# Optimization experiments

Measured on AMD Instinct MI355X. Metric: run time of the kernel, lower is better.

## Reference

```python
import jax, jax.numpy as jnp
import numpy as np
from jax import lax


def _l2n(t, eps=1e-12):
    n = jnp.sqrt(jnp.sum(t * t, axis=-1, keepdims=True))
    return t / jnp.maximum(n, eps)


def _ln(t, w, b, eps=1e-5):
    mu = jnp.mean(t, -1, keepdims=True)
    var = jnp.var(t, -1, keepdims=True)
    return (t - mu) / jnp.sqrt(var + eps) * w + b


def _unfold3(x):
    # nn.Unfold(kernel_size=3, padding=1, stride=1): [B,C,H,W] -> [B,C,9,H*W]
    B, C, H, W = x.shape
    xp = jnp.pad(x, ((0, 0), (0, 0), (1, 1), (1, 1)))
    pat = jnp.stack([xp[:, :, i:i + H, j:j + W] for i in range(3) for j in range(3)], axis=2)
    return pat.reshape(B, C, 9, H * W)


def _forward(x, norm1_w, norm1_b, q_w, q_b, kv_w, kv_b, temperature, query_embedding,
             learnable_tokens, learnable_bias, sr_w, sr_b, pln_w, pln_b, proj_w, proj_b,
             norm2_w, norm2_b, fc1_w, fc1_b, dw_w, dw_b, fc2_w, fc2_b):
    B, C, H, W = x.shape
    nh = temperature.shape[0]
    d = C // nh
    N = H * W
    K = 9  # local_len = window_size**2
    # norm1 (WithBias LayerNorm over channel dim, channels-last)
    y = _ln(x.reshape(B, C, N).transpose(0, 2, 1), norm1_w, norm1_b)  # [B,N,C]
    # ---- AggregatedAttention ----
    q = (y @ q_w.T + q_b).reshape(B, N, nh, d).transpose(0, 2, 1, 3)  # [B,h,N,d]
    qn = _l2n(q)
    qs = (qn + query_embedding) * jax.nn.softplus(temperature)
    kv = y @ kv_w.T + kv_b  # [B,N,2C]
    k_loc = _l2n(kv[..., :C].reshape(B, N, nh, d)).reshape(B, N, C)
    kvl = jnp.concatenate([k_loc, kv[..., C:]], -1).transpose(0, 2, 1).reshape(B, 2 * C, H, W)
    pat = _unfold3(kvl).reshape(B, 2 * nh, d, K, N).transpose(0, 1, 4, 2, 3)  # [B,2h,N,d,K]
    k_l, v_l = pat[:, :nh], pat[:, nh:]
    attn_local = jnp.einsum('bhnd,bhndk->bhnk', qs, k_l)  # [B,h,N,K]
    # pooled branch; sr_ratio=1 so adaptive_avg_pool2d is identity
    y4 = y.transpose(0, 2, 1).reshape(B, C, H, W)
    xp = jax.nn.gelu(jnp.einsum('oc,bchw->bohw', sr_w, y4) + sr_b[:, None, None], approximate=False)
    xp = _ln(xp.reshape(B, C, N).transpose(0, 2, 1), pln_w, pln_b)  # [B,pool_len,C]
    kvp = (xp @ kv_w.T + kv_b).reshape(B, N, 2 * nh, d).transpose(0, 2, 1, 3)
    k_p = _l2n(kvp[:, :nh])
    v_p = kvp[:, nh:]
    attn_pool = jnp.einsum('bhnd,bhmd->bhnm', qs, k_p)  # [B,h,N,pool_len]
    attn = jax.nn.softmax(jnp.concatenate([attn_local, attn_pool], -1), axis=-1)
    a_l, a_p = attn[..., :K], attn[..., K:]
    w_l = jnp.einsum('bhnd,hdk->bhnk', qn, learnable_tokens) + learnable_bias + a_l
    x_local = jnp.einsum('bhnk,bhndk->bhnd', w_l, v_l)
    x_pool = jnp.einsum('bhnm,bhmd->bhnd', a_p, v_p)
    xo = (x_local + x_pool).transpose(0, 2, 1, 3).reshape(B, N, C)
    # proj then raw torch-style reshape [B,N,C] -> [B,C,H,W] (memory reinterpretation)
    xo = (xo @ proj_w.T + proj_b).reshape(B, C, H, W)
    x = x + xo
    # ---- ConvolutionalGLU MLP ----
    hf = dw_b.shape[0]
    y2 = _ln(x.reshape(B, C, N).transpose(0, 2, 1), norm2_w, norm2_b).transpose(0, 2, 1).reshape(B, C, H, W)
    f1 = jnp.einsum('oc,bchw->bohw', fc1_w, y2) + fc1_b[:, None, None]
    a, v = f1[:, :hf], f1[:, hf:]
    dw = lax.conv_general_dilated(a, dw_w, (1, 1), ((1, 1), (1, 1)),
                                  feature_group_count=hf,
                                  dimension_numbers=('NCHW', 'OIHW', 'NCHW')) + dw_b[:, None, None]
    g = jax.nn.gelu(dw, approximate=False) * v
    out = jnp.einsum('oc,bchw->bohw', fc2_w, g) + fc2_b[:, None, None]
    return x + out


def setup_inputs() -> dict:
    key = jax.random.key(0)
    B, C, H, W = 2, 128, 56, 56
    nh, d, K = 4, 32, 9
    hf = int(2 * int(C * 4.0) / 3)  # 341
    ks = iter(jax.random.split(key, 16))
    rn = lambda shape, s=0.02: jax.random.normal(next(ks), shape, jnp.float32) * s
    return {
        'x': jax.random.normal(next(ks), (B, C, H, W), jnp.float32),
        'norm1_w': jnp.ones((C,), jnp.float32), 'norm1_b': jnp.zeros((C,), jnp.float32),
        'q_w': rn((C, C)), 'q_b': jnp.zeros((C,), jnp.float32),
        'kv_w': rn((2 * C, C)), 'kv_b': jnp.zeros((2 * C,), jnp.float32),
        'temperature': jnp.full((nh, 1, 1), float(np.log(np.exp(1.0 / 0.24) - 1.0)), jnp.float32),
        'query_embedding': rn((nh, 1, d)),
        'learnable_tokens': rn((nh, d, K)),
        'learnable_bias': jnp.zeros((nh, 1, K), jnp.float32),
        'sr_w': rn((C, C)), 'sr_b': jnp.zeros((C,), jnp.float32),
        'pln_w': jnp.ones((C,), jnp.float32), 'pln_b': jnp.zeros((C,), jnp.float32),
        'proj_w': rn((C, C)), 'proj_b': jnp.zeros((C,), jnp.float32),
        'norm2_w': jnp.ones((C,), jnp.float32), 'norm2_b': jnp.zeros((C,), jnp.float32),
        'fc1_w': rn((2 * hf, C)), 'fc1_b': jnp.zeros((2 * hf,), jnp.float32),
        'dw_w': rn((hf, 1, 3, 3)), 'dw_b': jnp.zeros((hf,), jnp.float32),
        'fc2_w': rn((C, hf)), 'fc2_b': jnp.zeros((C,), jnp.float32),
    }


def reference(x, norm1_w, norm1_b, q_w, q_b, kv_w, kv_b, temperature, query_embedding,
              learnable_tokens, learnable_bias, sr_w, sr_b, pln_w, pln_b, proj_w, proj_b,
              norm2_w, norm2_b, fc1_w, fc1_b, dw_w, dw_b, fc2_w, fc2_b):
    return _forward(x, norm1_w, norm1_b, q_w, q_b, kv_w, kv_b, temperature, query_embedding,
                    learnable_tokens, learnable_bias, sr_w, sr_b, pln_w, pln_b, proj_w, proj_b,
                    norm2_w, norm2_b, fc1_w, fc1_b, dw_w, dw_b, fc2_w, fc2_b)
```

## Files before the change

### kernel.cpp

```cpp
#include <hip/hip_runtime.h>
#include <hip/hip_bf16.h>

typedef __hip_bfloat16 bf16;
typedef short s8v __attribute__((ext_vector_type(8)));
typedef short s4v __attribute__((ext_vector_type(4)));
typedef float f4v __attribute__((ext_vector_type(4)));

#define DEVI __device__ __forceinline__

DEVI float cvt(float x){ return x; }
DEVI float cvt(bf16 x){ return __bfloat162float(x); }

DEVI void stg(float* p, float v){ *p = v; }
DEVI void stg(bf16* p, float v){ *p = __float2bfloat16(v); }

DEVI float gelu_exact(float x){
  return 0.5f*x*(1.0f + erff(x*0.70710678118654752440f));
}

constexpr int B_ = 2, C_ = 128, H_ = 56, W_ = 56, N_ = 3136, NH_ = 4, D_ = 32, HF_ = 341;
constexpr int ROWS_ = B_*N_;
constexpr int KF2 = 352;
constexpr int GQ_ = NH_*B_*N_;
constexpr int FW = 512;
constexpr int KSP = 12;
constexpr int SPLIT = 256;
constexpr int NTILE = 392;
constexpr float LOG2E = 1.4426950408889634f;
constexpr float E8L2  = 11.541560327111707f;

DEVI void ln_tile_body(int tile, int t, const float* __restrict__ x,
                       const float* __restrict__ w, const float* __restrict__ bia,
                       bf16* __restrict__ y, float* sm , float* st )
{
  int b = tile / 196, nb = (tile % 196) * 16;
  {
    int c = t >> 1, half = t & 1;
    const float* xp = x + ((long)b*C_ + c)*N_ + nb + half*8;
    f4v v0 = *(const f4v*)xp;
    f4v v1 = *(const f4v*)(xp + 4);
    #pragma unroll
    for (int j=0;j<4;j++){
      sm[c*17 + half*8 + j    ] = v0[j];
      sm[c*17 + half*8 + 4 + j] = v1[j];
    }
  }
  __syncthreads();
  {
    int i = t >> 4, k = t & 15;
    float s = 0.f, ss = 0.f;
    #pragma unroll
    for (int u=0;u<8;u++){
      float v = sm[(k + u*16)*17 + i];
      s += v; ss = fmaf(v,v,ss);
    }
    #pragma unroll
    for (int off=1; off<16; off<<=1){
      s  += __shfl_xor(s,  off);
      ss += __shfl_xor(ss, off);
    }
    if (k == 0){
      float mu  = s*(1.0f/128.0f);
      float var = fmaxf(ss*(1.0f/128.0f) - mu*mu, 0.f);
      st[i]      = mu;
      st[16 + i] = rsqrtf(var + 1e-5f);
    }
  }
  __syncthreads();
  {
    int i = t >> 4, c0 = (t & 15)*8;
    float mu = st[i], inv = st[16 + i];
    bf16 o8[8];
    #pragma unroll
    for (int j=0;j<8;j++){
      int c = c0 + j;
      o8[j] = __float2bfloat16((sm[c*17 + i] - mu)*inv*w[c] + bia[c]);
    }
    *(s8v*)(y + ((long)(b*N_ + nb + i))*C_ + c0) = *(const s8v*)o8;
  }
}

__global__ __launch_bounds__(256)
void ln_tile_kernel(const float* __restrict__ x, const float* __restrict__ w,
                    const float* __restrict__ bia, bf16* __restrict__ y)
{
  __shared__ float sm[128*17];
  __shared__ float st[32];
  ln_tile_body(blockIdx.x, threadIdx.x, x, w, bia, y, sm, st);
}

__global__ __launch_bounds__(256)
void head_kernel(const float* __restrict__ q_w, const float* __restrict__ kv_w,
                 const float* __restrict__ sr_w, const float* __restrict__ proj_w,
                 const float* __restrict__ fc1_w, const float* __restrict__ fc2_w,
                 const float* __restrict__ q_b, const float* __restrict__ kv_b,
                 const float* __restrict__ sr_b,
                 bf16* __restrict__ out, float* __restrict__ bias_out,
                 const float* __restrict__ x_in, const float* __restrict__ n1w,
                 const float* __restrict__ n1b, bf16* __restrict__ y)
{
  __shared__ float sm[128*17];
  __shared__ float st[32];
  if (blockIdx.x >= 839){
    ln_tile_body(blockIdx.x - 839, threadIdx.x, x_in, n1w, n1b, y, sm, st);
    return;
  }
  int t = blockIdx.x*256 + threadIdx.x;
  if (t >= 214272){
    int i = t - 214272;
    if (i < 512){
      float bv = (i < 128) ? q_b[i] : (i < 384) ? kv_b[i-128] : sr_b[i-384];
      bias_out[i] = bv;
    }
    return;
  }
  float v;
  if      (t <  16384) v = q_w[t];
  else if (t <  49152) v = kv_w[t-16384];
  else if (t <  65536) v = sr_w[t-49152];
  else if (t <  81920) v = proj_w[t-65536];
  else if (t < 169216) v = fc1_w[t-81920];
  else {
    int i = t - 169216; int m = i / KF2, kp = i % KF2;
    v = (kp < HF_) ? fc2_w[m*HF_ + kp] : 0.f;
  }
  out[t] = __float2bfloat16(v);
}

template<int KT, int MODE, typename TC, int BM=64, int LDA=KT, int NCH=1>
__global__ __launch_bounds__(256)
void gemm_mfma(const bf16* __restrict__ A, const bf16* __restrict__ B,
               const float* __restrict__ bias, const float* __restrict__ res,
               TC* __restrict__ Cm, int M, int Nn,
               long sA, long sB, long sC, long sR,
               const float* __restrict__ qe, const float* __restrict__ temp,
               bf16* __restrict__ aux0, bf16* __restrict__ aux1)
{
  A  += (long)blockIdx.z * sA;
  B  += (long)blockIdx.z * sB;
  Cm += (long)blockIdx.z * sC;
  if (res) res += (long)blockIdx.z * sR;
  int lane = threadIdx.x & 63, w = threadIdx.x >> 6;
  int m = lane & 15, quad = lane >> 4;
  int n0 = blockIdx.x*64, m0 = blockIdx.y*BM;
  const bf16* ap[NCH];
  #pragma unroll
  for (int cc=0; cc<NCH; cc++){
    int ar = m0 + cc*64 + w*16 + m;
    if (ar >= M) ar = M-1;
    ap[cc] = A + (long)ar*LDA + quad*8;
  }
  const bf16* bp = B + (long)(n0 + m)*KT + quad*8;
  s8v a4[KT/32];
  if (MODE==7){
    float s=0.f, ssum=0.f;
    #pragma unroll
    for (int i=0;i<KT/32;i++){
      a4[i] = *(const s8v*)(ap[0] + i*32);
      #pragma unroll
      for (int j=0;j<8;j++){
        float v = cvt(((const bf16*)&a4[i])[j]);
        s += v; ssum = fmaf(v,v,ssum);
      }
    }
    s    += __shfl_xor(s,16);    s    += __shfl_xor(s,32);
    ssum += __shfl_xor(ssum,16); ssum += __shfl_xor(ssum,32);
    float mu  = s*(1.0f/128.0f);
    float var = fmaxf(ssum*(1.0f/128.0f) - mu*mu, 0.f);
    float inv = rsqrtf(var + 1e-5f);
    #pragma unroll
    for (int i=0;i<KT/32;i++){
      #pragma unroll
      for (int j=0;j<8;j++){
        int c = i*32 + quad*8 + j;
        float v = cvt(((const bf16*)&a4[i])[j]);
        ((bf16*)&a4[i])[j] = __float2bfloat16((v-mu)*inv*qe[c] + temp[c]);
      }
    }
  }
  f4v acc[NCH][4];
  #pragma unroll
  for (int cc=0; cc<NCH; cc++)
    #pragma unroll
    for (int s=0;s<4;s++) acc[cc][s] = (f4v){0.f,0.f,0.f,0.f};
  #pragma unroll
  for (int k0 = 0; k0 < KT; k0 += 32){
    s8v bf[4];
    #pragma unroll
    for (int s=0;s<4;s++) bf[s] = *(const s8v*)(bp + (long)s*16*KT + k0);
    #pragma unroll
    for (int cc=0; cc<NCH; cc++){
      s8v af = (MODE==7) ? a4[k0/32] : *(const s8v*)(ap[cc] + k0);
      #pragma unroll
      for (int s=0;s<4;s++)
        acc[cc][s] = __builtin_amdgcn_mfma_f32_16x16x32_bf16(af, bf[s], acc[cc][s], 0, 0, 0);
    }
  }
  if ((MODE==6 || MODE==7) && blockIdx.x < 2){
    int hA = blockIdx.x*2, hB = hA+1;
    float spA = 0.f, spB = 0.f;
    if (MODE==6){
      spA = log1pf(expf(temp[hA])) * LOG2E;
      spB = log1pf(expf(temp[hB])) * LOG2E;
    }
    #pragma unroll
    for (int cc=0; cc<NCH; cc++){
      #pragma unroll
      for (int r=0;r<4;r++){
        float v4[4];
        #pragma unroll
        for (int s=0;s<4;s++) v4[s] = acc[cc][s][r] + bias[n0 + s*16 + m];
        float ssA = v4[0]*v4[0] + v4[1]*v4[1];
        float ssB = v4[2]*v4[2] + v4[3]*v4[3];
        #pragma unroll
        for (int off=1; off<16; off<<=1){
          ssA += __shfl_xor(ssA, off);
          ssB += __shfl_xor(ssB, off);
        }
        float invA = 1.f/fmaxf(sqrtf(ssA), 1e-12f);
        float invB = 1.f/fmaxf(sqrtf(ssB), 1e-12f);
        int gm = m0 + cc*64 + w*16 + quad*4 + r;
        int b = gm / N_, n = gm % N_;
        #pragma unroll
        for (int s=0;s<4;s++){
          int h = (s<2) ? hA : hB;
          int d = (s&1)*16 + m;
          float v = v4[s] * ((s<2) ? invA : invB);
          if (MODE==6) v = (v + qe[h*D_ + d]) * ((s<2) ? spA : spB);
          aux0[((long)(b*NH_+h)*N_ + n)*D_ + d] = __float2bfloat16(v);
        }
      }
    }
    return;
  }
  if (MODE==7){
    int gm0 = m0 + w*16 + quad*4;
    int b = gm0 / N_, nb = gm0 % N_;
    #pragma unroll
    for (int s=0;s<4;s++){
      int h = (blockIdx.x-2)*2 + (s>>1);
      int d = (s&1)*16 + m;
      bf16 p4[4];
      #pragma unroll
      for (int r=0;r<4;r++) p4[r] = __float2bfloat16(acc[0][s][r] + bias[n0 + s*16 + m]);
      *(s4v*)(aux1 + ((long)(b*NH_+h)*D_ + d)*N_ + nb) = *(const s4v*)p4;
    }
    return;
  }
  #pragma unroll
  for (int cc=0; cc<NCH; cc++){
    int m0c = m0 + cc*64;
    #pragma unroll
    for (int s=0;s<4;s++){
      int gn = n0 + s*16 + m;
      #pragma unroll
      for (int r=0;r<4;r++){
        int gm = m0c + w*16 + quad*4 + r;
        if (gm >= M) continue;
        float v = acc[cc][s][r];
        if (MODE==1 || MODE==4 || MODE==6) v += bias[gn];
        else                               v += bias[gm];
        if (MODE==6 && gn >= 384) v = gelu_exact(v);
        if (MODE==4 || MODE==5) v += res[(long)gm*Nn + gn];
        stg(&Cm[(long)gm*Nn + gn], v);
      }
    }
  }
}

__global__ __launch_bounds__(256)
void attn_part_kernel(const bf16* __restrict__ qs_, const bf16* __restrict__ kp_,
                      const bf16* __restrict__ vp_,
                      bf16* __restrict__ Op, float* __restrict__ Lp)
{
  int bh = blockIdx.y;
  int z  = blockIdx.z;
  int lane = threadIdx.x & 63;
  int w    = threadIdx.x >> 6;
  int m    = lane & 15, quad = lane >> 4;
  int base = blockIdx.x*256 + w*16;

  s8v af[4]; bool hasQ[4];
  #pragma unroll
  for (int ch=0; ch<4; ch++){
    int qq = base + ch*64;
    hasQ[ch] = (qq < N_);
    af[ch] = *(const s8v*)(qs_ + ((long)bh*N_ + (hasQ[ch] ? qq : base) + m)*D_ + quad*8);
  }
  const bf16* kpb = kp_ + (long)bh*N_*D_;
  const bf16* vpb = vp_ + (long)bh*D_*N_;
  int kperm = (m & 3) + 8*(m >> 2);
  f4v o0[4], o1[4];
  float l[4];
  #pragma unroll
  for (int ch=0; ch<4; ch++){
    o0[ch] = (f4v){0.f,0.f,0.f,0.f}; o1[ch] = (f4v){0.f,0.f,0.f,0.f};
    l[ch] = 0.f;
  }

  auto loadKV = [&](s8v* kf, s8v* vf, int t){
    kf[0] = *(const s8v*)(kpb + (long)(t + kperm     )*D_ + quad*8);
    kf[1] = *(const s8v*)(kpb + (long)(t + kperm +  4)*D_ + quad*8);
    kf[2] = *(const s8v*)(kpb + (long)(t + kperm + 32)*D_ + quad*8);
    kf[3] = *(const s8v*)(kpb + (long)(t + kperm + 36)*D_ + quad*8);
    vf[0] = *(const s8v*)(vpb + (long)(m     )*N_ + t      + quad*8);
    vf[1] = *(const s8v*)(vpb + (long)(16 + m)*N_ + t      + quad*8);
    vf[2] = *(const s8v*)(vpb + (long)(m     )*N_ + t + 32 + quad*8);
    vf[3] = *(const s8v*)(vpb + (long)(16 + m)*N_ + t + 32 + quad*8);
  };
  auto compute = [&](const s8v* kf, const s8v* vf){
    __builtin_amdgcn_s_setprio(1);
    #pragma unroll
    for (int ch=0; ch<4; ch++){
      f4v c[4];
      #pragma unroll
      for (int s=0;s<4;s++){
        c[s] = (f4v){-E8L2, -E8L2, -E8L2, -E8L2};
        c[s] = __builtin_amdgcn_mfma_f32_16x16x32_bf16(kf[s], af[ch], c[s], 0, 0, 0);
      }
      bf16 p8a[8], p8b[8];
      float ls = 0.f;
      #pragma unroll
      for (int r=0;r<4;r++){
        float ea = __builtin_amdgcn_exp2f(c[0][r]);
        float eb = __builtin_amdgcn_exp2f(c[1][r]);
        float ec = __builtin_amdgcn_exp2f(c[2][r]);
        float ed = __builtin_amdgcn_exp2f(c[3][r]);
        ls += (ea+eb) + (ec+ed);
        p8a[r] = __float2bfloat16(ea); p8a[4+r] = __float2bfloat16(eb);
        p8b[r] = __float2bfloat16(ec); p8b[4+r] = __float2bfloat16(ed);
      }
      l[ch] += ls;
      s8v pa = *(const s8v*)p8a, pb = *(const s8v*)p8b;
      o0[ch] = __builtin_amdgcn_mfma_f32_16x16x32_bf16(pa, vf[0], o0[ch], 0, 0, 0);
      o1[ch] = __builtin_amdgcn_mfma_f32_16x16x32_bf16(pa, vf[1], o1[ch], 0, 0, 0);
      o0[ch] = __builtin_amdgcn_mfma_f32_16x16x32_bf16(pb, vf[2], o0[ch], 0, 0, 0);
      o1[ch] = __builtin_amdgcn_mfma_f32_16x16x32_bf16(pb, vf[3], o1[ch], 0, 0, 0);
    }
    __builtin_amdgcn_s_setprio(0);
  };

  int tlo = z*SPLIT, thi = (z==KSP-1) ? N_ : tlo + SPLIT;
  s8v kfA[4], vfA[4], kfB[4], vfB[4];
  int t0 = tlo;
  loadKV(kfA, vfA, t0);
  for (;;){
    if (t0 + 64 < thi) loadKV(kfB, vfB, t0 + 64);
    compute(kfA, vfA);
    t0 += 64;
    if (t0 >= thi) break;
    if (t0 + 64 < thi) loadKV(kfA, vfA, t0 + 64);
    compute(kfB, vfB);
    t0 += 64;
    if (t0 >= thi) break;
  }
  #pragma unroll
  for (int ch=0; ch<4; ch++){
    if (!hasQ[ch]) continue;
    float lr = l[ch];
    lr += __shfl_xor(lr, 16);
    lr += __shfl_xor(lr, 32);
    long gqBase = (long)bh*N_ + base + ch*64;
    #pragma unroll
    for (int r=0;r<4;r++){
      bf16* op = Op + ((long)z*GQ_ + gqBase + quad*4 + r)*32;
      op[m]      = __float2bfloat16(o0[ch][r]);
      op[16 + m] = __float2bfloat16(o1[ch][r]);
    }
    if (quad == 0) Lp[(long)z*GQ_ + gqBase + m] = lr;
  }
}

__global__ __launch_bounds__(256)
void attn_combine_kernel(const bf16* __restrict__ Op, const float* __restrict__ Lp,
                         const bf16* __restrict__ qs_, const bf16* __restrict__ fused,
                         const float* __restrict__ qe, const float* __restrict__ temp,
                         const float* __restrict__ tokens, const float* __restrict__ tbias,
                         bf16* __restrict__ xo)
{
  int t  = blockIdx.x*256 + threadIdx.x;
  int gq = t >> 3;
  int l8 = t & 7;
  int d0 = l8*4;
  int n = gq % N_; int bh = gq / N_; int h = bh & 3; int b = bh >> 2;
  float out[4] = {0.f,0.f,0.f,0.f};
  #pragma unroll
  for (int z=0; z<KSP; z++){
    s4v o4 = *(const s4v*)(Op + ((long)z*GQ_ + gq)*32 + d0);
    #pragma unroll
    for (int j=0;j<4;j++) out[j] += cvt(((const bf16*)&o4)[j]);
  }
  float L = 0.f;
  for (int z=l8; z<KSP; z+=8) L += Lp[(long)z*GQ_ + gq];
  #pragma unroll
  for (int off=1; off<8; off<<=1) L += __shfl_xor(L, off);
  float q[4];
  {
    s4v q4 = *(const s4v*)(qs_ + (long)gq*D_ + d0);
    #pragma unroll
    for (int j=0;j<4;j++) q[j] = cvt(((const bf16*)&q4)[j]) * 0.6931471805599453f;
  }
  int hy = n / W_, wx = n % W_;
  const bf16* kvb = fused + (long)b*N_*FW + 128 + h*D_ + d0;
  float sl[9];
  #pragma unroll
  for (int k=0;k<9;k++){
    int di = k/3-1, dj = k%3-1;
    int yy = hy+di, xx = wx+dj;
    bool ok = (yy>=0 && yy<H_ && xx>=0 && xx<W_);
    float dot = 0.f, ss = 0.f;
    if (ok){
      s4v k4 = *(const s4v*)(kvb + (long)(yy*W_+xx)*FW);
      #pragma unroll
      for (int j=0;j<4;j++){
        float kk = cvt(((const bf16*)&k4)[j]);
        dot = fmaf(q[j], kk, dot);
        ss  = fmaf(kk, kk, ss);
      }
    }
    #pragma unroll
    for (int off=1; off<8; off<<=1){
      dot += __shfl_xor(dot, off);
      ss  += __shfl_xor(ss,  off);
    }
    sl[k] = ok ? dot / fmaxf(sqrtf(ss), 1e-12f) : 0.f;
  }
  #pragma unroll
  for (int k=0;k<9;k++) L += __expf(sl[k] - 8.f);
  float invL = 1.f/L;
  #pragma unroll
  for (int j=0;j<4;j++) out[j] *= invL;
  float sp = log1pf(expf(temp[h]));
  float invsp = 1.f/sp;
  float qn[4];
  #pragma unroll
  for (int j=0;j<4;j++) qn[j] = q[j]*invsp - qe[h*D_ + d0 + j];
  #pragma unroll
  for (int k=0;k<9;k++){
    float tok = 0.f;
    #pragma unroll
    for (int j=0;j<4;j++) tok = fmaf(qn[j], tokens[(h*D_ + d0 + j)*9 + k], tok);
    #pragma unroll
    for (int off=1; off<8; off<<=1) tok += __shfl_xor(tok, off);
    float wl = tok + tbias[h*9+k] + __expf(sl[k] - 8.f)*invL;
    int di = k/3-1, dj = k%3-1;
    int yy = hy+di, xx = wx+dj;
    if (yy>=0 && yy<H_ && xx>=0 && xx<W_){
      s4v v4 = *(const s4v*)(kvb + (long)(yy*W_+xx)*FW + 128);
      #pragma unroll
      for (int j=0;j<4;j++) out[j] = fmaf(wl, cvt(((const bf16*)&v4)[j]), out[j]);
    }
  }
  bf16 o4[4];
  #pragma unroll
  for (int j=0;j<4;j++) o4[j] = __float2bfloat16(out[j]);
  *(s4v*)(xo + ((long)(b*N_ + n))*C_ + h*D_ + d0) = *(const s4v*)o4;
}

__global__ __launch_bounds__(256)
void dwconv_kernel(const bf16* __restrict__ f1, const float* __restrict__ dww,
                   const float* __restrict__ dwb, bf16* __restrict__ g)
{
  int t = blockIdx.x*256 + threadIdx.x;
  int b = t / (352*392); int r = t - b*(352*392);
  int c = r / 392, chunk = r - c*392;
  int y = chunk / 7, x0 = (chunk - y*7)*8;
  f1 += (long)b*2*HF_*N_;
  bf16* gb = g + (long)b*N_*KF2 + c;
  if (c >= HF_){
    #pragma unroll
    for (int j=0;j<8;j++) gb[(long)(y*W_ + x0 + j)*KF2] = __float2bfloat16(0.f);
    return;
  }
  const bf16* ap = f1 + (long)c*N_;
  float acc[8];
  #pragma unroll
  for (int j=0;j<8;j++) acc[j] = dwb[c];
  #pragma unroll
  for (int dy=-1; dy<=1; dy++){
    int yy = y + dy;
    if (yy < 0 || yy >= H_) continue;
    int base = yy*W_ + x0;
    s8v mid = *(const s8v*)(ap + base);
    float wnd[10];
    wnd[0] = (x0 > 0)      ? cvt(ap[base-1]) : 0.f;
    #pragma unroll
    for (int j=0;j<8;j++) wnd[1+j] = cvt(((const bf16*)&mid)[j]);
    wnd[9] = (x0 + 8 < W_) ? cvt(ap[base+8]) : 0.f;
    float k0 = dww[c*9 + (dy+1)*3    ];
    float k1 = dww[c*9 + (dy+1)*3 + 1];
    float k2 = dww[c*9 + (dy+1)*3 + 2];
    #pragma unroll
    for (int j=0;j<8;j++)
      acc[j] = fmaf(k0, wnd[j], fmaf(k1, wnd[j+1], fmaf(k2, wnd[j+2], acc[j])));
  }
  s8v g8 = *(const s8v*)(f1 + (long)(HF_+c)*N_ + y*W_ + x0);
  #pragma unroll
  for (int j=0;j<8;j++){
    float val = gelu_exact(acc[j]) * cvt(((const bf16*)&g8)[j]);
    gb[(long)(y*W_ + x0 + j)*KF2] = __float2bfloat16(val);
  }
}

extern "C" void kernel_launch(void* const* d_in, const int* in_sizes, int n_in,
                              void* d_out, int out_size, void* d_ws, size_t ws_size,
                              hipStream_t stream)
{
  (void)in_sizes; (void)n_in; (void)out_size; (void)ws_size;
  const float* x_in      = (const float*)d_in[0];
  const float* norm1_w   = (const float*)d_in[1];
  const float* norm1_b   = (const float*)d_in[2];
  const float* q_w       = (const float*)d_in[3];
  const float* q_b       = (const float*)d_in[4];
  const float* kv_w      = (const float*)d_in[5];
  const float* kv_b      = (const float*)d_in[6];
  const float* temp      = (const float*)d_in[7];
  const float* qe        = (const float*)d_in[8];
  const float* tokens    = (const float*)d_in[9];
  const float* tbias     = (const float*)d_in[10];
  const float* sr_w      = (const float*)d_in[11];
  const float* sr_b      = (const float*)d_in[12];
  const float* pln_w     = (const float*)d_in[13];
  const float* pln_b     = (const float*)d_in[14];
  const float* proj_w    = (const float*)d_in[15];
  const float* proj_b    = (const float*)d_in[16];
  const float* norm2_w   = (const float*)d_in[17];
  const float* norm2_b   = (const float*)d_in[18];
  const float* fc1_w     = (const float*)d_in[19];
  const float* fc1_b     = (const float*)d_in[20];
  const float* dw_w      = (const float*)d_in[21];
  const float* dw_b      = (const float*)d_in[22];
  const float* fc2_w     = (const float*)d_in[23];
  const float* fc2_b     = (const float*)d_in[24];

  char* w8 = (char*)d_ws;
  bf16*  fused   = (bf16*)(w8 + 0);
  float* x2      = (float*)(w8 + 0);
  bf16*  y2      = (bf16*)(w8 + 3211264);
  bf16*  f1b     = (bf16*)(w8 + 4816896);
  bf16*  qs      = (bf16*)(w8 + 6422528);
  bf16*  k_p     = (bf16*)(w8 + 9633792);
  bf16*  v_p     = (bf16*)(w8 + 11239424);
  bf16*  Opart   = (bf16*)(w8 + 13045056);
  bf16*  g_rows  = (bf16*)(w8 + 32312640);
  bf16*  wbase   = (bf16*)(w8 + 36728128);
  float* fbias   = (float*)(w8 + 37156672);
  bf16*  y       = f1b;
  bf16*  xo      = (bf16*)d_out;
  float* Lpart   = (float*)((char*)d_out + 1605632);
  bf16*  proj_wb = wbase + 65536;
  bf16*  fc1_wb  = wbase + 81920;
  bf16*  fc2_wb  = wbase + 169216;

  head_kernel<<<839 + NTILE, 256, 0, stream>>>(
      q_w, kv_w, sr_w, proj_w, fc1_w, fc2_w, q_b, kv_b, sr_b, wbase, fbias,
      x_in, norm1_w, norm1_b, y);
  gemm_mfma<128, 6, bf16, 128, 128, 2><<<dim3(8,49), 256, 0, stream>>>(
      y, wbase, fbias, nullptr, fused, ROWS_, FW, 0,0,0,0, qe, temp, qs, nullptr);
  gemm_mfma<128, 7, bf16, 64, FW><<<dim3(4,98), 256, 0, stream>>>(
      fused + 384, wbase + 16384, kv_b, nullptr, (bf16*)nullptr, ROWS_, 256, 0,0,0,0,
      pln_w, pln_b, k_p, v_p);
  attn_part_kernel<<<dim3(13,8,KSP), 256, 0, stream>>>(qs, k_p, v_p, Opart, Lpart);
  attn_combine_kernel<<<GQ_*8/256, 256, 0, stream>>>(Opart, Lpart, qs, fused,
                                                     qe, temp, tokens, tbias, xo);
  gemm_mfma<128, 4, float, 16><<<dim3(2,392), 64, 0, stream>>>(
      xo, proj_wb, proj_b, x_in, x2, ROWS_, 128, 0,0,0,0, nullptr, nullptr, nullptr, nullptr);
  ln_tile_kernel<<<NTILE, 256, 0, stream>>>(x2, norm2_w, norm2_b, y2);
  gemm_mfma<128, 3, bf16, 128, 128, 2><<<dim3(49,6,B_), 256, 0, stream>>>(
      fc1_wb, y2, fc1_b, nullptr, f1b, 2*HF_, N_,
      0, (long)N_*C_, (long)2*HF_*N_, 0, nullptr, nullptr, nullptr, nullptr);
  dwconv_kernel<<<(B_*352*392)/256, 256, 0, stream>>>(f1b, dw_w, dw_b, g_rows);
  gemm_mfma<KF2, 5, float, 16><<<dim3(49,8,B_), 64, 0, stream>>>(
      fc2_wb, g_rows, fc2_b, x2, (float*)d_out, C_, N_,
      0, (long)N_*KF2, (long)C_*N_, (long)C_*N_, nullptr, nullptr, nullptr, nullptr);
}
```

Measured before the change: 229.7 us.

## Vectorize weight cast, transpose dwconv output via LDS, retune attention split, set MFMA priority

```diff
diff --git a/kernel.cpp b/kernel.cpp
--- a/kernel.cpp
+++ b/kernel.cpp
@@ -23,8 +23,8 @@
 constexpr int KF2 = 352;
 constexpr int GQ_ = NH_*B_*N_;
 constexpr int FW = 512;
-constexpr int KSP = 12;
-constexpr int SPLIT = 256;
+constexpr int KSP = 8;
+constexpr int SPLIT = 384;
 constexpr int NTILE = 392;
 constexpr float LOG2E = 1.4426950408889634f;
 constexpr float E8L2  = 11.541560327111707f;
@@ -101,30 +101,37 @@
 {
   __shared__ float sm[128*17];
   __shared__ float st[32];
-  if (blockIdx.x >= 839){
-    ln_tile_body(blockIdx.x - 839, threadIdx.x, x_in, n1w, n1b, y, sm, st);
+  if (blockIdx.x >= 212){
+    ln_tile_body(blockIdx.x - 212, threadIdx.x, x_in, n1w, n1b, y, sm, st);
     return;
   }
   int t = blockIdx.x*256 + threadIdx.x;
-  if (t >= 214272){
-    int i = t - 214272;
-    if (i < 512){
-      float bv = (i < 128) ? q_b[i] : (i < 384) ? kv_b[i-128] : sr_b[i-384];
-      bias_out[i] = bv;
-    }
-    return;
-  }
-  float v;
-  if      (t <  16384) v = q_w[t];
-  else if (t <  49152) v = kv_w[t-16384];
-  else if (t <  65536) v = sr_w[t-49152];
-  else if (t <  81920) v = proj_w[t-65536];
-  else if (t < 169216) v = fc1_w[t-81920];
-  else {
-    int i = t - 169216; int m = i / KF2, kp = i % KF2;
-    v = (kp < HF_) ? fc2_w[m*HF_ + kp] : 0.f;
-  }
-  out[t] = __float2bfloat16(v);
+  if (t < 42304){
+    int t0 = t*4;
+    const float* src;
+    if      (t0 <  16384) src = q_w    + t0;
+    else if (t0 <  49152) src = kv_w   + (t0-16384);
+    else if (t0 <  65536) src = sr_w   + (t0-49152);
+    else if (t0 <  81920) src = proj_w + (t0-65536);
+    else                  src = fc1_w  + (t0-81920);
+    f4v v = *(const f4v*)src;
+    bf16 o4[4];
+    #pragma unroll
+    for (int j=0;j<4;j++) o4[j] = __float2bfloat16(v[j]);
+    *(s4v*)(out + t0) = *(const s4v*)o4;
+  } else if (t < 53568){
+    int i = (t - 42304)*4;
+    int m = i / KF2, kp = i % KF2;
+    bf16 o4[4];
+    #pragma unroll
+    for (int j=0;j<4;j++)
+      o4[j] = __float2bfloat16((kp+j < HF_) ? fc2_w[m*HF_ + kp + j] : 0.f);
+    *(s4v*)(out + 169216 + i) = *(const s4v*)o4;
+  } else if (t < 54080){
+    int i = t - 53568;
+    float bv = (i < 128) ? q_b[i] : (i < 384) ? kv_b[i-128] : sr_b[i-384];
+    bias_out[i] = bv;
+  }
 }
 
 template<int KT, int MODE, typename TC, int BM=64, int LDA=KT, int NCH=1>
@@ -183,6 +190,7 @@
   for (int cc=0; cc<NCH; cc++)
     #pragma unroll
     for (int s=0;s<4;s++) acc[cc][s] = (f4v){0.f,0.f,0.f,0.f};
+  __builtin_amdgcn_s_setprio(1);
   #pragma unroll
   for (int k0 = 0; k0 < KT; k0 += 32){
     s8v bf[4];
@@ -196,6 +204,7 @@
         acc[cc][s] = __builtin_amdgcn_mfma_f32_16x16x32_bf16(af, bf[s], acc[cc][s], 0, 0, 0);
     }
   }
+  __builtin_amdgcn_s_setprio(0);
   if ((MODE==6 || MODE==7) && blockIdx.x < 2){
     int hA = blockIdx.x*2, hB = hA+1;
     float spA = 0.f, spB = 0.f;
@@ -461,44 +470,60 @@
 void dwconv_kernel(const bf16* __restrict__ f1, const float* __restrict__ dww,
                    const float* __restrict__ dwb, bf16* __restrict__ g)
 {
-  int t = blockIdx.x*256 + threadIdx.x;
-  int b = t / (352*392); int r = t - b*(352*392);
-  int c = r / 392, chunk = r - c*392;
-  int y = chunk / 7, x0 = (chunk - y*7)*8;
+  __shared__ bf16 sg[32*72];
+  int bx = blockIdx.x;
+  int ntile = bx % 49;
+  int cg    = (bx / 49) % 11;
+  int b     = bx / (49*11);
+  int t = threadIdx.x;
   f1 += (long)b*2*HF_*N_;
-  bf16* gb = g + (long)b*N_*KF2 + c;
-  if (c >= HF_){
-    #pragma unroll
-    for (int j=0;j<8;j++) gb[(long)(y*W_ + x0 + j)*KF2] = __float2bfloat16(0.f);
-    return;
-  }
-  const bf16* ap = f1 + (long)c*N_;
-  float acc[8];
-  #pragma unroll
-  for (int j=0;j<8;j++) acc[j] = dwb[c];
-  #pragma unroll
-  for (int dy=-1; dy<=1; dy++){
-    int yy = y + dy;
-    if (yy < 0 || yy >= H_) continue;
-    int base = yy*W_ + x0;
-    s8v mid = *(const s8v*)(ap + base);
-    float wnd[10];
-    wnd[0] = (x0 > 0)      ? cvt(ap[base-1]) : 0.f;
-    #pragma unroll
-    for (int j=0;j<8;j++) wnd[1+j] = cvt(((const bf16*)&mid)[j]);
-    wnd[9] = (x0 + 8 < W_) ? cvt(ap[base+8]) : 0.f;
-    float k0 = dww[c*9 + (dy+1)*3    ];
-    float k1 = dww[c*9 + (dy+1)*3 + 1];
-    float k2 = dww[c*9 + (dy+1)*3 + 2];
-    #pragma unroll
-    for (int j=0;j<8;j++)
-      acc[j] = fmaf(k0, wnd[j], fmaf(k1, wnd[j+1], fmaf(k2, wnd[j+2], acc[j])));
-  }
-  s8v g8 = *(const s8v*)(f1 + (long)(HF_+c)*N_ + y*W_ + x0);
-  #pragma unroll
-  for (int j=0;j<8;j++){
-    float val = gelu_exact(acc[j]) * cvt(((const bf16*)&g8)[j]);
-    gb[(long)(y*W_ + x0 + j)*KF2] = __float2bfloat16(val);
+  {
+    int c_local = t & 31, chun = t >> 5;
+    int c = cg*32 + c_local;
+    int n0 = ntile*64 + chun*8;
+    int y = n0 / W_, x0 = n0 % W_;
+    bf16 o8[8];
+    if (c < HF_){
+      const bf16* ap = f1 + (long)c*N_;
+      float acc[8];
+      #pragma unroll
+      for (int j=0;j<8;j++) acc[j] = dwb[c];
+      #pragma unroll
+      for (int dy=-1; dy<=1; dy++){
+        int yy = y + dy;
+        if (yy < 0 || yy >= H_) continue;
+        int base = yy*W_ + x0;
+        s8v mid = *(const s8v*)(ap + base);
+        float wnd[10];
+        wnd[0] = (x0 > 0)      ? cvt(ap[base-1]) : 0.f;
+        #pragma unroll
+        for (int j=0;j<8;j++) wnd[1+j] = cvt(((const bf16*)&mid)[j]);
+        wnd[9] = (x0 + 8 < W_) ? cvt(ap[base+8]) : 0.f;
+        float k0 = dww[c*9 + (dy+1)*3    ];
+        float k1 = dww[c*9 + (dy+1)*3 + 1];
+        float k2 = dww[c*9 + (dy+1)*3 + 2];
+        #pragma unroll
+        for (int j=0;j<8;j++)
+          acc[j] = fmaf(k0, wnd[j], fmaf(k1, wnd[j+1], fmaf(k2, wnd[j+2], acc[j])));
+      }
+      s8v g8 = *(const s8v*)(f1 + (long)(HF_+c)*N_ + n0);
+      #pragma unroll
+      for (int j=0;j<8;j++)
+        o8[j] = __float2bfloat16(gelu_exact(acc[j]) * cvt(((const bf16*)&g8)[j]));
+    } else {
+      #pragma unroll
+      for (int j=0;j<8;j++) o8[j] = __float2bfloat16(0.f);
+    }
+    *(s8v*)(&sg[c_local*72 + chun*8]) = *(const s8v*)o8;
+  }
+  __syncthreads();
+  {
+    int n_local = t >> 2, c0 = (t & 3)*8;
+    bf16 o8[8];
+    #pragma unroll
+    for (int j=0;j<8;j++) o8[j] = sg[(c0+j)*72 + n_local];
+    *(s8v*)(g + (long)b*N_*KF2 + (long)(ntile*64 + n_local)*KF2 + cg*32 + c0)
+        = *(const s8v*)o8;
   }
 }
 
@@ -552,7 +577,7 @@
   bf16*  fc1_wb  = wbase + 81920;
   bf16*  fc2_wb  = wbase + 169216;
 
-  head_kernel<<<839 + NTILE, 256, 0, stream>>>(
+  head_kernel<<<212 + NTILE, 256, 0, stream>>>(
       q_w, kv_w, sr_w, proj_w, fc1_w, fc2_w, q_b, kv_b, sr_b, wbase, fbias,
       x_in, norm1_w, norm1_b, y);
   gemm_mfma<128, 6, bf16, 128, 128, 2><<<dim3(8,49), 256, 0, stream>>>(
@@ -569,7 +594,7 @@
   gemm_mfma<128, 3, bf16, 128, 128, 2><<<dim3(49,6,B_), 256, 0, stream>>>(
       fc1_wb, y2, fc1_b, nullptr, f1b, 2*HF_, N_,
       0, (long)N_*C_, (long)2*HF_*N_, 0, nullptr, nullptr, nullptr, nullptr);
-  dwconv_kernel<<<(B_*352*392)/256, 256, 0, stream>>>(f1b, dw_w, dw_b, g_rows);
+  dwconv_kernel<<<B_*11*49, 256, 0, stream>>>(f1b, dw_w, dw_b, g_rows);
   gemm_mfma<KF2, 5, float, 16><<<dim3(49,8,B_), 64, 0, stream>>>(
       fc2_wb, g_rows, fc2_b, x2, (float*)d_out, C_, N_,
       0, (long)N_*KF2, (long)C_*N_, (long)C_*N_, nullptr, nullptr, nullptr, nullptr);
```

Result: faster. 222.3 us (-3.2%).
